# Kernel tuning notes

Measured on AMD Instinct MI355X. Metric: run time of the kernel, lower is better.

Reference implementation:

```python
import jax, jax.numpy as jnp
import numpy as np

B, N, C_IN, C_OUT, H = 8, 1024, 256, 512, 8
DH = C_OUT // H  # per-head dim
LN_EPS = 1e-5


def setup_inputs() -> dict:
    key = jax.random.key(0)
    ks = jax.random.split(key, 8)
    # xavier_normal std for [in, out] fan pair
    std = float(np.sqrt(2.0 / (C_IN + DH)))
    x = jax.random.normal(ks[0], (B, N, C_IN), dtype=jnp.float32)
    adj = jax.random.uniform(ks[1], (B, N, N), dtype=jnp.float32)
    W_q = jax.random.normal(ks[2], (H, C_IN, DH), dtype=jnp.float32) * std
    W_k = jax.random.normal(ks[3], (H, C_IN, DH), dtype=jnp.float32) * std
    W_v = jax.random.normal(ks[4], (H, C_IN, DH), dtype=jnp.float32) * std
    # Conv1d(in, out, kernel=1) == pointwise linear: weight [out, in], bias [out]
    bound = float(1.0 / np.sqrt(C_IN))
    conv_w = jax.random.uniform(ks[5], (C_OUT, C_IN), dtype=jnp.float32, minval=-bound, maxval=bound)
    conv_b = jax.random.uniform(ks[6], (C_OUT,), dtype=jnp.float32, minval=-bound, maxval=bound)
    ln_w = jnp.ones((C_OUT,), dtype=jnp.float32)
    ln_b = jnp.zeros((C_OUT,), dtype=jnp.float32)
    return {"x": x, "adj": adj, "W_q": W_q, "W_k": W_k, "W_v": W_v,
            "conv_w": conv_w, "conv_b": conv_b, "ln_w": ln_w, "ln_b": ln_b}


def reference(x, adj, W_q, W_k, W_v, conv_w, conv_b, ln_w, ln_b):
    # NOTE: in the original module, adj is used only to compute D_neg/A_hat,
    # which are discarded; it has no effect on the output. Attention is dense.
    dh = W_q.shape[-1]
    scale = 1.0 / jnp.sqrt(jnp.asarray(dh, dtype=x.dtype))
    # batched per-head projections: [B,N,Cin] x [H,Cin,dh] -> [B,H,N,dh]
    Q = jnp.einsum('bni,hio->bhno', x, W_q)
    K = jnp.einsum('bni,hio->bhno', x, W_k)
    V = jnp.einsum('bni,hio->bhno', x, W_v)
    scores = jnp.einsum('bhqd,bhkd->bhqk', Q, K) * scale  # [B,H,N,N]
    attn = jax.nn.softmax(scores, axis=-1)
    out = jax.nn.relu(jnp.einsum('bhqk,bhkd->bhqd', attn, V))  # [B,H,N,dh]
    b, h, n, d = out.shape
    out = out.transpose(0, 2, 1, 3).reshape(b, n, h * d)  # concat heads -> [B,N,Cout]
    # matching_conv: 1x1 conv == linear over channels
    proj = jnp.einsum('bni,oi->bno', x, conv_w) + conv_b
    y = out + proj
    mean = jnp.mean(y, axis=-1, keepdims=True)
    var = jnp.var(y, axis=-1, keepdims=True)
    y = (y - mean) * jax.lax.rsqrt(var + LN_EPS)
    return y * ln_w + ln_b
```

## Files before the change

### kernel.cpp

```cpp
#include <hip/hip_runtime.h>

#define B_ 8
#define N_ 1024
#define CIN_ 256
#define COUT_ 512
#define H_ 8
#define DH_ 64

typedef __attribute__((ext_vector_type(8))) short bf8;
typedef __attribute__((ext_vector_type(4))) short s4;
typedef __attribute__((ext_vector_type(4))) float f4;
typedef __attribute__((ext_vector_type(2))) unsigned int u2;

__device__ __forceinline__ short f2bf(float f) {
  unsigned u = __builtin_bit_cast(unsigned, f);
  u += 0x7fffu + ((u >> 16) & 1u);
  return (short)(u >> 16);
}
__device__ __forceinline__ float bf2f(short s) {
  unsigned u = ((unsigned)(unsigned short)s) << 16;
  return __builtin_bit_cast(float, u);
}

#if __has_builtin(__builtin_amdgcn_exp2f)
#define EXP2 __builtin_amdgcn_exp2f
#else
#define EXP2 exp2f
#endif

__device__ __forceinline__ unsigned cvtpk(float a, float b) {
  unsigned u;
  asm("v_cvt_pk_bf16_f32 %0, %1, %2" : "=v"(u) : "v"(a), "v"(b));
  return u;
}

#define MFMA16(a, b, c) __builtin_amdgcn_mfma_f32_16x16x32_bf16((a), (b), (c), 0, 0, 0)

#define GLD16(gp, lp)                                                              \
  __builtin_amdgcn_global_load_lds((const __attribute__((address_space(1))) void*)(gp), \
                                   (__attribute__((address_space(3))) void*)(lp), 16, 0, 0)

__global__ void k_prep(const float* __restrict__ Wq, const float* __restrict__ Wk,
                       const float* __restrict__ Wv, const float* __restrict__ Cw,
                       const float* __restrict__ x, short* __restrict__ Wt,
                       short* __restrict__ xb) {
  int blk = blockIdx.x;
  if (blk < 2048) {
    int col = blk;
    int k = threadIdx.x;
    float v;
    if (col < 512) {
      int h = col >> 6, d = col & 63;
      v = Wq[(h * CIN_ + k) * DH_ + d];
    } else if (col < 1024) {
      int c = col - 512, h = c >> 6, d = c & 63;
      v = Wk[(h * CIN_ + k) * DH_ + d];
    } else if (col < 1536) {
      int c = col - 1024, h = c >> 6, d = c & 63;
      v = Wv[(h * CIN_ + k) * DH_ + d];
    } else {
      v = Cw[(col - 1536) * CIN_ + k];
    }
    Wt[col * CIN_ + k] = f2bf(v);
  } else {
    int i = (blk - 2048) * 256 + threadIdx.x;
    f4 a = *reinterpret_cast<const f4*>(x + (size_t)i * 8);
    f4 b = *reinterpret_cast<const f4*>(x + (size_t)i * 8 + 4);
    bf8 o;
    o[0] = f2bf(a[0]); o[1] = f2bf(a[1]); o[2] = f2bf(a[2]); o[3] = f2bf(a[3]);
    o[4] = f2bf(b[0]); o[5] = f2bf(b[1]); o[6] = f2bf(b[2]); o[7] = f2bf(b[3]);
    *reinterpret_cast<bf8*>(xb + (size_t)i * 8) = o;
  }
}

__global__ __launch_bounds__(256) void k_gemm(const short* __restrict__ xb, const short* __restrict__ Wt,
                                              short* __restrict__ Qw, short* __restrict__ Kw,
                                              short* __restrict__ Vt, short* __restrict__ Pj) {
  __shared__ short Al[2][128][64];
  __shared__ short Bl[2][128][64];
  int tid = threadIdx.x;
  int mt = blockIdx.x >> 4, nt = blockIdx.x & 15;
  int row0 = mt * 128, col0 = nt * 128;
  int w = tid >> 6, lane = tid & 63, g = lane >> 4, lr = lane & 15;
  int wm = w >> 1, wn = w & 1;
  f4 acc[4][4];
#pragma unroll
  for (int i = 0; i < 4; ++i)
#pragma unroll
    for (int j = 0; j < 4; ++j) acc[i][j] = (f4){0.f, 0.f, 0.f, 0.f};

  int srow[4], sgc[4];
#pragma unroll
  for (int p = 0; p < 4; ++p) {
    int s = p * 256 + tid;
    srow[p] = s >> 3;
    sgc[p] = (s & 7) ^ (srow[p] & 7);
  }

#define STAGE_AB(k0_, buf_)                                                     \
  {                                                                             \
    char* abase = (char*)&Al[buf_][0][0];                                       \
    char* bbase = (char*)&Bl[buf_][0][0];                                       \
    _Pragma("unroll")                                                           \
    for (int p = 0; p < 4; ++p) {                                               \
      int lb = (p * 256 + w * 64) << 4;                                         \
      GLD16(xb + (row0 + srow[p]) * CIN_ + (k0_) + sgc[p] * 8, abase + lb);     \
      GLD16(Wt + (col0 + srow[p]) * CIN_ + (k0_) + sgc[p] * 8, bbase + lb);     \
    }                                                                           \
  }

  STAGE_AB(0, 0);

  for (int kt = 0; kt < 4; ++kt) {
    int cur = kt & 1;
    if (kt < 3) {
      STAGE_AB((kt + 1) * 64, cur ^ 1);
      asm volatile("s_waitcnt vmcnt(8)" ::: "memory");
    } else {
      asm volatile("s_waitcnt vmcnt(0)" ::: "memory");
    }
    __builtin_amdgcn_s_barrier();

    const short* al = &Al[cur][0][0];
    const short* bl = &Bl[cur][0][0];
    bf8 af[4][2], bb[4][2];
#pragma unroll
    for (int mi = 0; mi < 4; ++mi) {
      int R = wm * 64 + mi * 16 + lr;
      int sw = R & 7;
      af[mi][0] = *reinterpret_cast<const bf8*>(al + R * 64 + ((g ^ sw) * 8));
      af[mi][1] = *reinterpret_cast<const bf8*>(al + R * 64 + (((4 + g) ^ sw) * 8));
    }
#pragma unroll
    for (int ni = 0; ni < 4; ++ni) {
      int R = wn * 64 + ni * 16 + lr;
      int sw = R & 7;
      bb[ni][0] = *reinterpret_cast<const bf8*>(bl + R * 64 + ((g ^ sw) * 8));
      bb[ni][1] = *reinterpret_cast<const bf8*>(bl + R * 64 + (((4 + g) ^ sw) * 8));
    }
#pragma unroll
    for (int mi = 0; mi < 4; ++mi)
#pragma unroll
      for (int ni = 0; ni < 4; ++ni) {
        acc[mi][ni] = MFMA16(af[mi][0], bb[ni][0], acc[mi][ni]);
        acc[mi][ni] = MFMA16(af[mi][1], bb[ni][1], acc[mi][ni]);
      }
    asm volatile("s_waitcnt lgkmcnt(0)" ::: "memory");
    __builtin_amdgcn_s_barrier();
  }

  const float QSCL = 0.125f * 1.4426950408889634f;
#pragma unroll
  for (int mi = 0; mi < 4; ++mi)
#pragma unroll
    for (int ni = 0; ni < 4; ++ni) {
      int c = col0 + wn * 64 + ni * 16 + lr;
      int r0 = row0 + wm * 64 + mi * 16 + g * 4;
      int b = r0 >> 10, n0 = r0 & 1023;
      if (c < 1024) {
#pragma unroll
        for (int j = 0; j < 4; ++j) {
          int n = n0 + j;
          if (c < 512) {
            Qw[((b * H_ + (c >> 6)) * N_ + n) * DH_ + (c & 63)] = f2bf(acc[mi][ni][j] * QSCL);
          } else {
            int cc = c - 512;
            Kw[((b * H_ + (cc >> 6)) * N_ + n) * DH_ + (cc & 63)] = f2bf(acc[mi][ni][j]);
          }
        }
      } else if (c < 1536) {
        int cc = c - 1024;
        int hh = cc >> 6, d = cc & 63;
        s4 vv;
#pragma unroll
        for (int j = 0; j < 4; ++j) vv[j] = f2bf(acc[mi][ni][j]);
        *reinterpret_cast<s4*>(Vt + ((size_t)(b * H_ + hh) * DH_ + d) * N_ + n0) = vv;
      } else {
#pragma unroll
        for (int j = 0; j < 4; ++j) {
          Pj[(size_t)(r0 + j) * COUT_ + (c - 1536)] = f2bf(acc[mi][ni][j]);
        }
      }
    }
}

__global__ __launch_bounds__(256) void k_attn(const short* __restrict__ Qw, const short* __restrict__ Kw,
                                              const short* __restrict__ Vt, short* __restrict__ At) {
  __shared__ short Kl[4][64][64];
  __shared__ short Vl[4][64][64];
  __shared__ short Pl[4][2][16][64];
  int tid = threadIdx.x;
  int nid = ((blockIdx.x & 7) << 6) | (blockIdx.x >> 3);
  int bh = nid >> 3;
  int qb = nid & 7;
  int w = tid >> 6, lane = tid & 63, g = lane >> 4, lr = lane & 15;
  int qglob = qb * 128 + w * 32;
  const short* Qp = Qw + ((size_t)bh * N_ + qglob) * DH_;
  const short* Kp = Kw + (size_t)bh * N_ * DH_;
  const short* Vp = Vt + (size_t)bh * DH_ * N_;

  int sr0 = tid >> 3, sc0 = (tid & 7) ^ (sr0 & 7);
  int s1 = tid + 256;
  int sr1 = s1 >> 3, sc1 = (s1 & 7) ^ (sr1 & 7);
  int lo0 = (w * 64) << 4;
  int lo1 = (w * 64 + 256) << 4;

#define STAGE_KV(tt_, buf_)                                                     \
  {                                                                             \
    const short* kb = Kp + (tt_) * (64 * DH_);                                  \
    const short* vb = Vp + (tt_) * 64;                                          \
    char* klb = (char*)&Kl[buf_][0][0];                                         \
    char* vlb = (char*)&Vl[buf_][0][0];                                         \
    GLD16(kb + sr0 * 64 + sc0 * 8, klb + lo0);                                  \
    GLD16(kb + sr1 * 64 + sc1 * 8, klb + lo1);                                  \
    GLD16(vb + (size_t)sr0 * N_ + sc0 * 8, vlb + lo0);                          \
    GLD16(vb + (size_t)sr1 * N_ + sc1 * 8, vlb + lo1);                          \
  }

  STAGE_KV(0, 0);
  STAGE_KV(1, 1);

  bf8 aq[2][2];
#pragma unroll
  for (int qs = 0; qs < 2; ++qs) {
    aq[qs][0] = *reinterpret_cast<const bf8*>(Qp + (qs * 16 + lr) * DH_ + g * 8);
    aq[qs][1] = *reinterpret_cast<const bf8*>(Qp + (qs * 16 + lr) * DH_ + 32 + g * 8);
  }

  f4 o[2][4];
  f4 lacc[2];
#pragma unroll
  for (int qs = 0; qs < 2; ++qs) {
    lacc[qs] = (f4){0.f, 0.f, 0.f, 0.f};
#pragma unroll
    for (int i = 0; i < 4; ++i) o[qs][i] = (f4){0.f, 0.f, 0.f, 0.f};
  }

  const int swz = (lr & 7) << 3;
  short* pl0 = &Pl[w][0][0][0];
  short* pl1 = &Pl[w][1][0][0];

  for (int t = 0; t < 16; ++t) {
    int cur = t & 3;
    if (t < 14) {
      STAGE_KV(t + 2, (t + 2) & 3);
      asm volatile("s_waitcnt vmcnt(8)" ::: "memory");
    } else if (t == 14) {
      asm volatile("s_waitcnt vmcnt(4)" ::: "memory");
    } else {
      asm volatile("s_waitcnt vmcnt(0)" ::: "memory");
    }
    __builtin_amdgcn_s_barrier();

    const short* klc = &Kl[cur][0][0];
    bf8 bk0[4], bk1[4];
#pragma unroll
    for (int kt = 0; kt < 4; ++kt) {
      int R = kt * 16 + lr;
      const short* kr = klc + R * 64;
      int sw = (R & 7) << 3;
      bk0[kt] = *reinterpret_cast<const bf8*>(kr + ((g * 8) ^ sw));
      bk1[kt] = *reinterpret_cast<const bf8*>(kr + ((32 + g * 8) ^ sw));
    }
    f4 s0[4], s1v[4];
    __builtin_amdgcn_s_setprio(1);
#pragma unroll
    for (int kt = 0; kt < 4; ++kt) {
      f4 z = (f4){0.f, 0.f, 0.f, 0.f};
      z = MFMA16(bk0[kt], aq[0][0], z);
      z = MFMA16(bk1[kt], aq[0][1], z);
      s0[kt] = z;
      f4 z2 = (f4){0.f, 0.f, 0.f, 0.f};
      z2 = MFMA16(bk0[kt], aq[1][0], z2);
      z2 = MFMA16(bk1[kt], aq[1][1], z2);
      s1v[kt] = z2;
    }
    __builtin_amdgcn_s_setprio(0);
#pragma unroll
    for (int kt = 0; kt < 4; ++kt) {
      f4 p;
      p[0] = EXP2(s0[kt][0]); p[1] = EXP2(s0[kt][1]);
      p[2] = EXP2(s0[kt][2]); p[3] = EXP2(s0[kt][3]);
      lacc[0] += p;
      u2 pk;
      pk[0] = cvtpk(p[0], p[1]);
      pk[1] = cvtpk(p[2], p[3]);
      *reinterpret_cast<u2*>(pl0 + lr * 64 + ((kt * 16 + g * 4) ^ swz)) = pk;
    }
#pragma unroll
    for (int kt = 0; kt < 4; ++kt) {
      f4 p;
      p[0] = EXP2(s1v[kt][0]); p[1] = EXP2(s1v[kt][1]);
      p[2] = EXP2(s1v[kt][2]); p[3] = EXP2(s1v[kt][3]);
      lacc[1] += p;
      u2 pk;
      pk[0] = cvtpk(p[0], p[1]);
      pk[1] = cvtpk(p[2], p[3]);
      *reinterpret_cast<u2*>(pl1 + lr * 64 + ((kt * 16 + g * 4) ^ swz)) = pk;
    }
    asm volatile("s_waitcnt lgkmcnt(0)" ::: "memory");
    __builtin_amdgcn_sched_barrier(0);
    bf8 pa00 = *reinterpret_cast<const bf8*>(pl0 + lr * 64 + ((g * 8) ^ swz));
    bf8 pa01 = *reinterpret_cast<const bf8*>(pl0 + lr * 64 + ((32 + g * 8) ^ swz));
    bf8 pa10 = *reinterpret_cast<const bf8*>(pl1 + lr * 64 + ((g * 8) ^ swz));
    bf8 pa11 = *reinterpret_cast<const bf8*>(pl1 + lr * 64 + ((32 + g * 8) ^ swz));
    const short* vlc = &Vl[cur][0][0];
#pragma unroll
    for (int dt = 0; dt < 4; ++dt) {
      int R = dt * 16 + lr;
      const short* vr = vlc + R * 64;
      int sw = (R & 7) << 3;
      bf8 bv0 = *reinterpret_cast<const bf8*>(vr + ((g * 8) ^ sw));
      bf8 bv1 = *reinterpret_cast<const bf8*>(vr + ((32 + g * 8) ^ sw));
      __builtin_amdgcn_s_setprio(1);
      o[0][dt] = MFMA16(pa00, bv0, o[0][dt]);
      o[0][dt] = MFMA16(pa01, bv1, o[0][dt]);
      o[1][dt] = MFMA16(pa10, bv0, o[1][dt]);
      o[1][dt] = MFMA16(pa11, bv1, o[1][dt]);
      __builtin_amdgcn_s_setprio(0);
    }
    asm volatile("s_waitcnt lgkmcnt(0)" ::: "memory");
  }

  float ls[2];
#pragma unroll
  for (int qs = 0; qs < 2; ++qs) {
    float v = (lacc[qs][0] + lacc[qs][1]) + (lacc[qs][2] + lacc[qs][3]);
    v += __shfl_xor(v, 16, 64);
    v += __shfl_xor(v, 32, 64);
    ls[qs] = v;
  }
  float lf[2][4];
#pragma unroll
  for (int qs = 0; qs < 2; ++qs)
#pragma unroll
    for (int j = 0; j < 4; ++j)
      lf[qs][j] = __shfl(ls[qs], (lane & 48) + ((lane & 48) >> 2) + j, 64);
  int b = bh >> 3, h = bh & 7;
#pragma unroll
  for (int qs = 0; qs < 2; ++qs)
#pragma unroll
    for (int dt = 0; dt < 4; ++dt)
#pragma unroll
      for (int j = 0; j < 4; ++j) {
        float v = fmaxf(o[qs][dt][j] / lf[qs][j], 0.f);
        int n = qglob + qs * 16 + g * 4 + j;
        At[((size_t)b * N_ + n) * COUT_ + h * DH_ + dt * 16 + lr] = f2bf(v);
      }
}

__global__ __launch_bounds__(256) void k_ln(const short* __restrict__ At, const short* __restrict__ Pj,
                                            const float* __restrict__ cb, const float* __restrict__ lw,
                                            const float* __restrict__ lb, float* __restrict__ out) {
  int row = blockIdx.x * 4 + (threadIdx.x >> 6);
  int lane = threadIdx.x & 63;
  int c0 = lane * 8;
  bf8 a8 = *reinterpret_cast<const bf8*>(At + (size_t)row * COUT_ + c0);
  bf8 p8 = *reinterpret_cast<const bf8*>(Pj + (size_t)row * COUT_ + c0);
  float y[8];
  float sum = 0.f, sq = 0.f;
#pragma unroll
  for (int j = 0; j < 8; ++j) {
    float v = bf2f(a8[j]) + bf2f(p8[j]) + cb[c0 + j];
    y[j] = v;
    sum += v;
    sq += v * v;
  }
#pragma unroll
  for (int off = 1; off < 64; off <<= 1) {
    sum += __shfl_xor(sum, off, 64);
    sq += __shfl_xor(sq, off, 64);
  }
  float mean = sum * (1.f / 512.f);
  float var = sq * (1.f / 512.f) - mean * mean;
  float rstd = rsqrtf(var + 1e-5f);
  f4 o0, o1;
#pragma unroll
  for (int j = 0; j < 4; ++j) o0[j] = (y[j] - mean) * rstd * lw[c0 + j] + lb[c0 + j];
#pragma unroll
  for (int j = 0; j < 4; ++j) o1[j] = (y[4 + j] - mean) * rstd * lw[c0 + 4 + j] + lb[c0 + 4 + j];
  *reinterpret_cast<f4*>(out + (size_t)row * COUT_ + c0) = o0;
  *reinterpret_cast<f4*>(out + (size_t)row * COUT_ + c0 + 4) = o1;
}

extern "C" void kernel_launch(void* const* d_in, const int* in_sizes, int n_in,
                              void* d_out, int out_size, void* d_ws, size_t ws_size,
                              hipStream_t stream) {
  const float* x  = (const float*)d_in[0];
  const float* Wq = (const float*)d_in[2];
  const float* Wk = (const float*)d_in[3];
  const float* Wv = (const float*)d_in[4];
  const float* Cw = (const float*)d_in[5];
  const float* cb = (const float*)d_in[6];
  const float* lw = (const float*)d_in[7];
  const float* lb = (const float*)d_in[8];
  float* out = (float*)d_out;
  char* ws = (char*)d_ws;
  short* xb = (short*)(ws);
  short* Wt = (short*)(ws + (size_t)4194304);
  short* Qw = (short*)(ws + (size_t)5242880);
  short* Kw = (short*)(ws + (size_t)13631488);
  short* Vt = (short*)(ws + (size_t)22020096);
  short* Pj = (short*)(ws + (size_t)30408704);
  short* At = (short*)(ws + (size_t)38797312);

  hipLaunchKernelGGL(k_prep, dim3(3072), dim3(256), 0, stream, Wq, Wk, Wv, Cw, x, Wt, xb);
  hipLaunchKernelGGL(k_gemm, dim3(1024), dim3(256), 0, stream, xb, Wt, Qw, Kw, Vt, Pj);
  hipLaunchKernelGGL(k_attn, dim3(512), dim3(256), 0, stream, Qw, Kw, Vt, At);
  hipLaunchKernelGGL(k_ln, dim3(2048), dim3(256), 0, stream, At, Pj, cb, lw, lb, out);
}
```

Measured before the change: 65.64 us.

## Feed P·V MFMA directly from score registers, dropping the LDS round trip

The probability tile is no longer written to LDS and read back. It is kept in registers and fed straight into 16x16x16 bf16 MFMAs, with V loaded in 4-element chunks that match the score-output layout. The output becomes transposed (query along lr), so the row-sum shuffle goes away and each lane writes 4 contiguous bf16 values instead of scattered scalars. The trade is twice as many MFMA instructions, each of half the K depth, and more, smaller V reads from LDS.

```diff
diff --git a/kernel.cpp b/kernel.cpp
--- a/kernel.cpp
+++ b/kernel.cpp
@@ -35,6 +35,8 @@
 }
 
 #define MFMA16(a, b, c) __builtin_amdgcn_mfma_f32_16x16x32_bf16((a), (b), (c), 0, 0, 0)
+
+#define MFMAPV(a, b, c) __builtin_amdgcn_mfma_f32_16x16x16bf16_1k((a), (b), (c), 0, 0, 0)
 
 #define GLD16(gp, lp)                                                              \
   __builtin_amdgcn_global_load_lds((const __attribute__((address_space(1))) void*)(gp), \
@@ -188,7 +190,6 @@
                                               const short* __restrict__ Vt, short* __restrict__ At) {
   __shared__ short Kl[4][64][64];
   __shared__ short Vl[4][64][64];
-  __shared__ short Pl[4][2][16][64];
   int tid = threadIdx.x;
   int nid = ((blockIdx.x & 7) << 6) | (blockIdx.x >> 3);
   int bh = nid >> 3;
@@ -236,10 +237,6 @@
     for (int i = 0; i < 4; ++i) o[qs][i] = (f4){0.f, 0.f, 0.f, 0.f};
   }
 
-  const int swz = (lr & 7) << 3;
-  short* pl0 = &Pl[w][0][0][0];
-  short* pl1 = &Pl[w][1][0][0];
-
   for (int t = 0; t < 16; ++t) {
     int cur = t & 3;
     if (t < 14) {
@@ -276,6 +273,7 @@
       s1v[kt] = z2;
     }
     __builtin_amdgcn_s_setprio(0);
+    s4 pq0[4], pq1[4];
 #pragma unroll
     for (int kt = 0; kt < 4; ++kt) {
       f4 p;
@@ -285,7 +283,7 @@
       u2 pk;
       pk[0] = cvtpk(p[0], p[1]);
       pk[1] = cvtpk(p[2], p[3]);
-      *reinterpret_cast<u2*>(pl0 + lr * 64 + ((kt * 16 + g * 4) ^ swz)) = pk;
+      pq0[kt] = __builtin_bit_cast(s4, pk);
     }
 #pragma unroll
     for (int kt = 0; kt < 4; ++kt) {
@@ -296,27 +294,27 @@
       u2 pk;
       pk[0] = cvtpk(p[0], p[1]);
       pk[1] = cvtpk(p[2], p[3]);
-      *reinterpret_cast<u2*>(pl1 + lr * 64 + ((kt * 16 + g * 4) ^ swz)) = pk;
-    }
-    asm volatile("s_waitcnt lgkmcnt(0)" ::: "memory");
-    __builtin_amdgcn_sched_barrier(0);
-    bf8 pa00 = *reinterpret_cast<const bf8*>(pl0 + lr * 64 + ((g * 8) ^ swz));
-    bf8 pa01 = *reinterpret_cast<const bf8*>(pl0 + lr * 64 + ((32 + g * 8) ^ swz));
-    bf8 pa10 = *reinterpret_cast<const bf8*>(pl1 + lr * 64 + ((g * 8) ^ swz));
-    bf8 pa11 = *reinterpret_cast<const bf8*>(pl1 + lr * 64 + ((32 + g * 8) ^ swz));
+      pq1[kt] = __builtin_bit_cast(s4, pk);
+    }
+
     const short* vlc = &Vl[cur][0][0];
 #pragma unroll
     for (int dt = 0; dt < 4; ++dt) {
       int R = dt * 16 + lr;
       const short* vr = vlc + R * 64;
-      int sw = (R & 7) << 3;
-      bf8 bv0 = *reinterpret_cast<const bf8*>(vr + ((g * 8) ^ sw));
-      bf8 bv1 = *reinterpret_cast<const bf8*>(vr + ((32 + g * 8) ^ sw));
+      int swR = R & 7;
+      s4 va[4];
+#pragma unroll
+      for (int kt = 0; kt < 4; ++kt) {
+        int ch = (kt * 2 + (g >> 1)) ^ swR;
+        va[kt] = *reinterpret_cast<const s4*>(vr + ch * 8 + (g & 1) * 4);
+      }
       __builtin_amdgcn_s_setprio(1);
-      o[0][dt] = MFMA16(pa00, bv0, o[0][dt]);
-      o[0][dt] = MFMA16(pa01, bv1, o[0][dt]);
-      o[1][dt] = MFMA16(pa10, bv0, o[1][dt]);
-      o[1][dt] = MFMA16(pa11, bv1, o[1][dt]);
+#pragma unroll
+      for (int kt = 0; kt < 4; ++kt) {
+        o[0][dt] = MFMAPV(va[kt], pq0[kt], o[0][dt]);
+        o[1][dt] = MFMAPV(va[kt], pq1[kt], o[1][dt]);
+      }
       __builtin_amdgcn_s_setprio(0);
     }
     asm volatile("s_waitcnt lgkmcnt(0)" ::: "memory");
@@ -330,23 +328,20 @@
     v += __shfl_xor(v, 32, 64);
     ls[qs] = v;
   }
-  float lf[2][4];
-#pragma unroll
-  for (int qs = 0; qs < 2; ++qs)
-#pragma unroll
-    for (int j = 0; j < 4; ++j)
-      lf[qs][j] = __shfl(ls[qs], (lane & 48) + ((lane & 48) >> 2) + j, 64);
   int b = bh >> 3, h = bh & 7;
 #pragma unroll
-  for (int qs = 0; qs < 2; ++qs)
-#pragma unroll
-    for (int dt = 0; dt < 4; ++dt)
-#pragma unroll
-      for (int j = 0; j < 4; ++j) {
-        float v = fmaxf(o[qs][dt][j] / lf[qs][j], 0.f);
-        int n = qglob + qs * 16 + g * 4 + j;
-        At[((size_t)b * N_ + n) * COUT_ + h * DH_ + dt * 16 + lr] = f2bf(v);
-      }
+  for (int qs = 0; qs < 2; ++qs) {
+    float inv = 1.f / ls[qs];
+    int n = qglob + qs * 16 + lr;
+    short* dst = At + ((size_t)b * N_ + n) * COUT_ + h * DH_;
+#pragma unroll
+    for (int dt = 0; dt < 4; ++dt) {
+      s4 ov;
+#pragma unroll
+      for (int j = 0; j < 4; ++j) ov[j] = f2bf(fmaxf(o[qs][dt][j] * inv, 0.f));
+      *reinterpret_cast<s4*>(dst + dt * 16 + g * 4) = ov;
+    }
+  }
 }
 
 __global__ __launch_bounds__(256) void k_ln(const short* __restrict__ At, const short* __restrict__ Pj,
```

New measurement: 66.40 us. No clear change (+1.2%).
